# Performance work log

Hardware: AMD Instinct MI355X
Metric: run time of the kernel (lower is better)

## Reference

```python
import jax, jax.numpy as jnp
import numpy as np

POOL = 7  # pooling_size


def setup_inputs() -> dict:
    key = jax.random.key(0)
    k1, k2, k3 = jax.random.split(key, 3)
    H = W = 256
    C = 512
    N = 512  # num_roi / number of proposals
    feature_map = jax.random.normal(k1, (1, H, W, C), dtype=jnp.float32)
    # [x, y, w, h] integer boxes; x+w <= 256, y+h <= 256, w,h >= 1
    xy = jax.random.randint(k2, (N, 2), 0, 128, dtype=jnp.int32)
    wh = jax.random.randint(k3, (N, 2), 1, 128, dtype=jnp.int32)
    proposals = jnp.concatenate([xy, wh], axis=1)  # [N, 4]
    return {"feature_map": feature_map, "proposals": proposals}


def _axis_coords(start, size, pool):
    """Source sample coords for TF2 bilinear resize (half-pixel centers),
    for a crop beginning at `start` with extent `size`, resized to `pool`."""
    sizef = size.astype(jnp.float32)
    scale = sizef / pool
    s = (jnp.arange(pool, dtype=jnp.float32) + 0.5) * scale - 0.5
    s = jnp.clip(s, 0.0, jnp.maximum(sizef - 1.0, 0.0))
    i0 = jnp.floor(s).astype(jnp.int32)
    i1 = jnp.minimum(i0 + 1, size - 1)
    frac = s - i0.astype(jnp.float32)
    return start + i0, start + i1, frac


def _crop_resize(fm, box):
    # fm: [H, W, C]; box: [x, y, w, h] (int32 scalars, traced)
    x, y, w, h = box[0], box[1], box[2], box[3]
    y0, y1, fy = _axis_coords(y, h, POOL)
    x0, x1, fx = _axis_coords(x, w, POOL)
    wx = fx[None, :, None]
    wy = fy[:, None, None]
    r0 = fm[y0]  # [POOL, W, C]
    r1 = fm[y1]
    top = r0[:, x0] * (1.0 - wx) + r0[:, x1] * wx  # [POOL, POOL, C]
    bot = r1[:, x0] * (1.0 - wx) + r1[:, x1] * wx
    return top * (1.0 - wy) + bot * wy


def reference(feature_map, proposals):
    # feature_map: [1, H, W, C]; proposals: [N, 4] = [x, y, w, h]
    # Original loops over proposals, crops fm[:, y:y+h, x:x+w, :] and
    # bilinearly resizes to [POOL, POOL], then concatenates along batch.
    fm = feature_map[0]  # batch size 1, as in the original usage
    out = jax.vmap(lambda box: _crop_resize(fm, box))(proposals)
    return out  # [N, POOL, POOL, C]
```

## Files before the change

kernel.cpp:

```cpp
#include <hip/hip_runtime.h>


constexpr int FW = 256;
constexpr int FC = 512;

__device__ __forceinline__ void axis_coords(int start, int size, int p,
                                            int& c0, int& c1, float& frac) {
    float s = ((float)p + 0.5f) * ((float)size / 7.0f) - 0.5f;
    s = fminf(fmaxf(s, 0.0f), (float)(size - 1));
    int i0 = (int)s;
    int i1 = min(i0 + 1, size - 1);
    frac = s - (float)i0;
    c0 = start + i0;
    c1 = start + i1;
}

__global__ __launch_bounds__(128) void roi_align_kernel(
        const float* __restrict__ fm,
        const int*   __restrict__ props,
        float*       __restrict__ out) {
    const int blk = blockIdx.x;
    const int n   = blk / 49;
    const int rem = blk - n * 49;
    const int py  = rem / 7;
    const int px  = rem - py * 7;

    const int4 box = ((const int4*)props)[n];
    int x0, x1, y0, y1;
    float fx, fy;
    axis_coords(box.x, box.z, px, x0, x1, fx);
    axis_coords(box.y, box.w, py, y0, y1, fy);

    const float gx = 1.0f - fx, gy = 1.0f - fy;

    const float4* __restrict__ p00 = (const float4*)(fm + ((size_t)y0 * FW + x0) * FC);
    const float4* __restrict__ p01 = (const float4*)(fm + ((size_t)y0 * FW + x1) * FC);
    const float4* __restrict__ p10 = (const float4*)(fm + ((size_t)y1 * FW + x0) * FC);
    const float4* __restrict__ p11 = (const float4*)(fm + ((size_t)y1 * FW + x1) * FC);
    float4* __restrict__ po        = (float4*)(out + (size_t)blk * FC);

    const int c = threadIdx.x;
    const float4 v00 = p00[c];
    const float4 v01 = p01[c];
    const float4 v10 = p10[c];
    const float4 v11 = p11[c];

    float4 r;
    r.x = (v00.x * gx + v01.x * fx) * gy + (v10.x * gx + v11.x * fx) * fy;
    r.y = (v00.y * gx + v01.y * fx) * gy + (v10.y * gx + v11.y * fx) * fy;
    r.z = (v00.z * gx + v01.z * fx) * gy + (v10.z * gx + v11.z * fx) * fy;
    r.w = (v00.w * gx + v01.w * fx) * gy + (v10.w * gx + v11.w * fx) * fy;
    po[c] = r;
}

extern "C" void kernel_launch(void* const* d_in, const int* in_sizes, int n_in,
                              void* d_out, int out_size, void* d_ws, size_t ws_size,
                              hipStream_t stream) {
    const float* fm    = (const float*)d_in[0];
    const int*   props = (const int*)d_in[1];
    float*       out   = (float*)d_out;

    const int N = in_sizes[1] / 4;
    roi_align_kernel<<<N * 49, 128, 0, stream>>>(fm, props, out);
}
```

Measured before the change: 198.3 us.

## Process a full pooled row per block with batched loads and nontemporal stores

Each block now computes all 7 output columns of one pooled row instead of a single output cell, so the grid drops from N*49 to N*7 blocks. All 28 gathered float4 loads are issued up front to raise memory-level parallelism per thread, and outputs are written with nontemporal stores to avoid polluting cache. In exchange, register pressure rises and there are fewer blocks to spread across CUs.

```diff
diff --git a/kernel.cpp b/kernel.cpp
--- a/kernel.cpp
+++ b/kernel.cpp
@@ -3,6 +3,9 @@
 
 constexpr int FW = 256;
 constexpr int FC = 512;
+constexpr int FC4 = FC / 4;
+
+typedef float vfloat4 __attribute__((ext_vector_type(4)));
 
 __device__ __forceinline__ void axis_coords(int start, int size, int p,
                                             int& c0, int& c1, float& frac) {
@@ -15,42 +18,50 @@
     c1 = start + i1;
 }
 
-__global__ __launch_bounds__(128) void roi_align_kernel(
+__global__ __launch_bounds__(128) void roi_align_row_kernel(
         const float* __restrict__ fm,
         const int*   __restrict__ props,
         float*       __restrict__ out) {
     const int blk = blockIdx.x;
-    const int n   = blk / 49;
-    const int rem = blk - n * 49;
-    const int py  = rem / 7;
-    const int px  = rem - py * 7;
+    const int n   = blk / 7;
+    const int py  = blk - n * 7;
 
     const int4 box = ((const int4*)props)[n];
-    int x0, x1, y0, y1;
-    float fx, fy;
-    axis_coords(box.x, box.z, px, x0, x1, fx);
+
+    int y0, y1;
+    float fy;
     axis_coords(box.y, box.w, py, y0, y1, fy);
+    const float gy = 1.0f - fy;
 
-    const float gx = 1.0f - fx, gy = 1.0f - fy;
+    int   x0[7], x1[7];
+    float fx[7];
+#pragma unroll
+    for (int px = 0; px < 7; ++px)
+        axis_coords(box.x, box.z, px, x0[px], x1[px], fx[px]);
 
-    const float4* __restrict__ p00 = (const float4*)(fm + ((size_t)y0 * FW + x0) * FC);
-    const float4* __restrict__ p01 = (const float4*)(fm + ((size_t)y0 * FW + x1) * FC);
-    const float4* __restrict__ p10 = (const float4*)(fm + ((size_t)y1 * FW + x0) * FC);
-    const float4* __restrict__ p11 = (const float4*)(fm + ((size_t)y1 * FW + x1) * FC);
-    float4* __restrict__ po        = (float4*)(out + (size_t)blk * FC);
+    const vfloat4* __restrict__ r0 = (const vfloat4*)(fm + (size_t)y0 * FW * FC);
+    const vfloat4* __restrict__ r1 = (const vfloat4*)(fm + (size_t)y1 * FW * FC);
+    vfloat4* __restrict__ po = (vfloat4*)(out + ((size_t)n * 49 + (size_t)py * 7) * FC);
 
     const int c = threadIdx.x;
-    const float4 v00 = p00[c];
-    const float4 v01 = p01[c];
-    const float4 v10 = p10[c];
-    const float4 v11 = p11[c];
 
-    float4 r;
-    r.x = (v00.x * gx + v01.x * fx) * gy + (v10.x * gx + v11.x * fx) * fy;
-    r.y = (v00.y * gx + v01.y * fx) * gy + (v10.y * gx + v11.y * fx) * fy;
-    r.z = (v00.z * gx + v01.z * fx) * gy + (v10.z * gx + v11.z * fx) * fy;
-    r.w = (v00.w * gx + v01.w * fx) * gy + (v10.w * gx + v11.w * fx) * fy;
-    po[c] = r;
+    vfloat4 v00[7], v01[7], v10[7], v11[7];
+#pragma unroll
+    for (int px = 0; px < 7; ++px) {
+        v00[px] = r0[x0[px] * FC4 + c];
+        v01[px] = r0[x1[px] * FC4 + c];
+        v10[px] = r1[x0[px] * FC4 + c];
+        v11[px] = r1[x1[px] * FC4 + c];
+    }
+
+#pragma unroll
+    for (int px = 0; px < 7; ++px) {
+        const float fxp = fx[px], gxp = 1.0f - fx[px];
+        vfloat4 top = v00[px] * gxp + v01[px] * fxp;
+        vfloat4 bot = v10[px] * gxp + v11[px] * fxp;
+        vfloat4 r   = top * gy + bot * fy;
+        __builtin_nontemporal_store(r, &po[px * FC4 + c]);
+    }
 }
 
 extern "C" void kernel_launch(void* const* d_in, const int* in_sizes, int n_in,
@@ -61,5 +72,5 @@
     float*       out   = (float*)d_out;
 
     const int N = in_sizes[1] / 4;
-    roi_align_kernel<<<N * 49, 128, 0, stream>>>(fm, props, out);
+    roi_align_row_kernel<<<N * 7, 128, 0, stream>>>(fm, props, out);
 }
```

Result: no change. 198.0 us (-0.1%).
